# Kernel tuning notes

Hardware: AMD Instinct MI355X
Metric: run time of the kernel (lower is better)

## Reference

```python
import jax, jax.numpy as jnp
import numpy as np

HEADS = 8
IN_C = 256
MDL = 512
N = 4
L = 4096
NE = 65536  # avg degree 16


def setup_inputs() -> dict:
    key = jax.random.key(0)
    ks = jax.random.split(key, 14)
    f32 = jnp.float32
    s = 0.05
    return {
        "queries": jax.random.normal(ks[0], (N, L, IN_C), f32),
        "keys": jax.random.normal(ks[1], (N, L, IN_C), f32),
        "values": jax.random.normal(ks[2], (N, L, IN_C), f32),
        "adj": jax.random.randint(ks[3], (2, NE), 0, L, dtype=jnp.int32),
        "edge_pos_enc": jax.random.normal(ks[4], (N, HEADS, NE), f32),
        "Wq": jax.random.normal(ks[5], (IN_C, MDL), f32) * s,
        "bq": jnp.zeros((MDL,), f32),
        "Wk": jax.random.normal(ks[6], (IN_C, MDL), f32) * s,
        "bk": jnp.zeros((MDL,), f32),
        "Wv": jax.random.normal(ks[7], (IN_C, MDL), f32) * s,
        "bv": jnp.zeros((MDL,), f32),
        "Wo": jax.random.normal(ks[8], (MDL, MDL), f32) * s,
        "bo": jnp.zeros((MDL,), f32),
    }


def reference(queries, keys, values, adj, edge_pos_enc, Wq, bq, Wk, bk, Wv, bv, Wo, bo):
    n, l, _ = queries.shape
    h = HEADS
    e = MDL // h  # per-head dim
    temp = 1.0 / jnp.sqrt(jnp.asarray(e, queries.dtype))
    dst, src = adj[0], adj[1]

    def split(x):  # (n, l, mdl) -> (n*h, l, e)
        return x.reshape(n, l, h, e).transpose(0, 2, 1, 3).reshape(n * h, l, e)

    q = split(queries @ Wq + bq)
    k = split(keys @ Wk + bk)
    v = split(values @ Wv + bv)
    epe = edge_pos_enc.reshape(n * h, NE)

    def head(qh, kh, vh, eh):
        # qh,kh,vh: (l, e); eh: (Ne,)
        scores = temp * (jnp.sum(qh[dst] * kh[src], axis=-1) + eh)  # (Ne,)
        m = jax.ops.segment_max(scores, dst, num_segments=l)
        p = jnp.exp(scores - m[dst])
        z = jax.ops.segment_sum(p, dst, num_segments=l)
        alpha = p / z[dst]  # segment softmax keyed by dst (adj[0])
        return jax.ops.segment_sum(alpha[:, None] * vh[src], dst, num_segments=l)  # (l, e)

    out = jax.vmap(head)(q, k, v, epe)  # (n*h, l, e)
    out = out.reshape(n, h, l, e).transpose(0, 2, 1, 3).reshape(n, l, h * e)
    return out @ Wo + bo
```

## Files before the change

kernel.cpp:

```cpp
#include <hip/hip_runtime.h>
#include <hip/hip_bf16.h>
#include <math.h>
#include <stdint.h>

#define HEADS 8
#define IN_C  256
#define MDL   512
#define NB    4
#define LL    4096
#define NE    65536
#define EDIM  64
#define TEMP  0.125f

typedef __bf16 bf16x8 __attribute__((ext_vector_type(8)));
typedef float  f32x4  __attribute__((ext_vector_type(4)));
typedef short  short8 __attribute__((ext_vector_type(8)));

__device__ __forceinline__ void glds16(const void* g, void* l) {
    __builtin_amdgcn_global_load_lds(
        (const __attribute__((address_space(1))) void*)g,
        (__attribute__((address_space(3))) void*)l, 16, 0, 0);
}

__device__ __forceinline__ short8 cvt8(float4 a, float4 b) {
    union { short8 v; __hip_bfloat16 h[8]; } u;
    u.h[0] = __float2bfloat16(a.x); u.h[1] = __float2bfloat16(a.y);
    u.h[2] = __float2bfloat16(a.z); u.h[3] = __float2bfloat16(a.w);
    u.h[4] = __float2bfloat16(b.x); u.h[5] = __float2bfloat16(b.y);
    u.h[6] = __float2bfloat16(b.z); u.h[7] = __float2bfloat16(b.w);
    return u.v;
}

__global__ __launch_bounds__(256) void gemm_qkv(
    const float* __restrict__ A0, const float* __restrict__ A1,
    const float* __restrict__ A2,
    const __hip_bfloat16* __restrict__ B0, const __hip_bfloat16* __restrict__ B1,
    const __hip_bfloat16* __restrict__ B2,
    const float* __restrict__ b0, const float* __restrict__ b1,
    const float* __restrict__ b2,
    __hip_bfloat16* __restrict__ C0, __hip_bfloat16* __restrict__ C1,
    __hip_bfloat16* __restrict__ C2, int M, int N, int K)
{
    __shared__ __align__(16) __hip_bfloat16 As[128 * 64];
    __shared__ __align__(16) __hip_bfloat16 Bs[128 * 64];

    const int z = blockIdx.z;
    const float* A           = (z == 0) ? A0 : (z == 1) ? A1 : A2;
    const __hip_bfloat16* Bt = (z == 0) ? B0 : (z == 1) ? B1 : B2;
    const float* bias        = (z == 0) ? b0 : (z == 1) ? b1 : b2;
    __hip_bfloat16* C        = (z == 0) ? C0 : (z == 1) ? C1 : C2;

    const int tid  = threadIdx.x;
    const int lane = tid & 63;
    const int w    = tid >> 6;
    const int wr   = w >> 1, wc = w & 1;
    const int bm   = blockIdx.y * 128, bn = blockIdx.x * 128;

    const float*          gA[4];
    const __hip_bfloat16* gB[4];
    __hip_bfloat16* lAw[4];
    __hip_bfloat16* lB[4];
    #pragma unroll
    for (int it = 0; it < 4; it++) {
        int idx  = it * 256 + tid;
        int r    = idx >> 3;
        int cpos = idx & 7;
        int cdat = cpos ^ (r & 7);
        gA[it]  = A  + (size_t)(bm + r) * K + cdat * 8;
        gB[it]  = Bt + (size_t)(bn + r) * K + cdat * 8;
        lAw[it] = As + r * 64 + cpos * 8;
        lB[it]  = Bs + (size_t)(it * 256 + w * 64) * 8;
    }

    int fa[2][4], fb[2][4];
    #pragma unroll
    for (int kk = 0; kk < 2; kk++)
        #pragma unroll
        for (int i = 0; i < 4; i++) {
            int rA = wr * 64 + i * 16 + (lane & 15);
            int gc = kk * 4 + (lane >> 4);
            fa[kk][i] = rA * 64 + (gc ^ (rA & 7)) * 8;
            int rB = wc * 64 + i * 16 + (lane & 15);
            fb[kk][i] = rB * 64 + (gc ^ (rB & 7)) * 8;
        }

    f32x4 acc[4][4] = {};

    for (int k0 = 0; k0 < K; k0 += 64) {
        #pragma unroll
        for (int it = 0; it < 4; it++) glds16(gB[it] + k0, lB[it]);
        #pragma unroll
        for (int it = 0; it < 4; it++) {
            float4 a = *(const float4*)(gA[it] + k0);
            float4 b = *(const float4*)(gA[it] + k0 + 4);
            *(short8*)lAw[it] = cvt8(a, b);
        }
        __syncthreads();

        #pragma unroll
        for (int kk = 0; kk < 2; kk++) {
            bf16x8 av[4], bv[4];
            #pragma unroll
            for (int i = 0; i < 4; i++) av[i] = *(const bf16x8*)(As + fa[kk][i]);
            #pragma unroll
            for (int i = 0; i < 4; i++) bv[i] = *(const bf16x8*)(Bs + fb[kk][i]);
            #pragma unroll
            for (int mi = 0; mi < 4; mi++)
                #pragma unroll
                for (int ni = 0; ni < 4; ni++)
                    acc[mi][ni] = __builtin_amdgcn_mfma_f32_16x16x32_bf16(
                        av[mi], bv[ni], acc[mi][ni], 0, 0, 0);
        }
        __syncthreads();
    }

    #pragma unroll
    for (int mi = 0; mi < 4; mi++) {
        int row = bm + wr * 64 + mi * 16 + (lane >> 4) * 4;
        #pragma unroll
        for (int ni = 0; ni < 4; ni++) {
            int col = bn + wc * 64 + ni * 16 + (lane & 15);
            float bb = bias[col];
            #pragma unroll
            for (int j = 0; j < 4; j++)
                C[(size_t)(row + j) * N + col] = __float2bfloat16(acc[mi][ni][j] + bb);
        }
    }
}

__global__ __launch_bounds__(256) void gemm_out(
    const __hip_bfloat16* __restrict__ A, const __hip_bfloat16* __restrict__ Bt,
    const float* __restrict__ bias, float* __restrict__ C, int M, int N, int K)
{
    __shared__ __align__(16) __hip_bfloat16 As[128 * 64];
    __shared__ __align__(16) __hip_bfloat16 Bs[128 * 64];

    const int tid  = threadIdx.x;
    const int lane = tid & 63;
    const int w    = tid >> 6;
    const int wr   = w >> 1, wc = w & 1;
    const int bm   = blockIdx.y * 128, bn = blockIdx.x * 128;

    const __hip_bfloat16* gA[4];
    const __hip_bfloat16* gB[4];
    __hip_bfloat16* lA[4];
    __hip_bfloat16* lB[4];
    #pragma unroll
    for (int it = 0; it < 4; it++) {
        int idx = it * 256 + tid;
        int r = idx >> 3;
        int c = (idx & 7) ^ (r & 7);
        gA[it] = A  + (size_t)(bm + r) * K + c * 8;
        gB[it] = Bt + (size_t)(bn + r) * K + c * 8;
        lA[it] = As + (size_t)(it * 256 + w * 64) * 8;
        lB[it] = Bs + (size_t)(it * 256 + w * 64) * 8;
    }

    int fa[2][4], fb[2][4];
    #pragma unroll
    for (int kk = 0; kk < 2; kk++)
        #pragma unroll
        for (int i = 0; i < 4; i++) {
            int rA = wr * 64 + i * 16 + (lane & 15);
            int gc = kk * 4 + (lane >> 4);
            fa[kk][i] = rA * 64 + (gc ^ (rA & 7)) * 8;
            int rB = wc * 64 + i * 16 + (lane & 15);
            fb[kk][i] = rB * 64 + (gc ^ (rB & 7)) * 8;
        }

    f32x4 acc[4][4] = {};

    for (int k0 = 0; k0 < K; k0 += 64) {
        #pragma unroll
        for (int it = 0; it < 4; it++) {
            glds16(gA[it] + k0, lA[it]);
            glds16(gB[it] + k0, lB[it]);
        }
        __syncthreads();

        #pragma unroll
        for (int kk = 0; kk < 2; kk++) {
            bf16x8 av[4], bv[4];
            #pragma unroll
            for (int i = 0; i < 4; i++) av[i] = *(const bf16x8*)(As + fa[kk][i]);
            #pragma unroll
            for (int i = 0; i < 4; i++) bv[i] = *(const bf16x8*)(Bs + fb[kk][i]);
            #pragma unroll
            for (int mi = 0; mi < 4; mi++)
                #pragma unroll
                for (int ni = 0; ni < 4; ni++)
                    acc[mi][ni] = __builtin_amdgcn_mfma_f32_16x16x32_bf16(
                        av[mi], bv[ni], acc[mi][ni], 0, 0, 0);
        }
        __syncthreads();
    }

    #pragma unroll
    for (int mi = 0; mi < 4; mi++) {
        int row = bm + wr * 64 + mi * 16 + (lane >> 4) * 4;
        #pragma unroll
        for (int ni = 0; ni < 4; ni++) {
            int col = bn + wc * 64 + ni * 16 + (lane & 15);
            float bb = bias[col];
            #pragma unroll
            for (int j = 0; j < 4; j++)
                C[(size_t)(row + j) * N + col] = acc[mi][ni][j] + bb;
        }
    }
}

__global__ void count_edges(const int* __restrict__ dst, int* __restrict__ counts, int ne) {
    int e = blockIdx.x * blockDim.x + threadIdx.x;
    if (e < ne) atomicAdd(&counts[dst[e]], 1);
}

__global__ __launch_bounds__(1024) void scan_offsets(
    const int* __restrict__ counts, int* __restrict__ offsets,
    int* __restrict__ cursor, int* __restrict__ reorder)
{
    __shared__ int wsum[16];
    __shared__ int bcnt[9], boff[9];
    const int tid  = threadIdx.x;
    const int lane = tid & 63;
    const int wid  = tid >> 6;

    if (tid < 9) bcnt[tid] = 0;

    int c[4];
    int base = tid * 4;
    int s = 0;
    #pragma unroll
    for (int i = 0; i < 4; i++) { c[i] = counts[base + i]; s += c[i]; }

    int v = s;
    #pragma unroll
    for (int off = 1; off < 64; off <<= 1) {
        int t = __shfl_up(v, off);
        if (lane >= off) v += t;
    }
    if (lane == 63) wsum[wid] = v;
    __syncthreads();
    if (wid == 0) {
        int wv = (lane < 16) ? wsum[lane] : 0;
        #pragma unroll
        for (int off = 1; off < 16; off <<= 1) {
            int t = __shfl_up(wv, off);
            if (lane >= off) wv += t;
        }
        if (lane < 16) wsum[lane] = wv;
    }
    __syncthreads();

    int prefix = (wid > 0 ? wsum[wid - 1] : 0) + (v - s);
    int run = prefix;
    int mybk[4];
    #pragma unroll
    for (int i = 0; i < 4; i++) {
        offsets[base + i] = run;
        cursor[base + i]  = run;
        run += c[i];
        int sc = (c[i] + 7) >> 3; if (sc > 8) sc = 8;
        mybk[i] = 8 - sc;
        atomicAdd(&bcnt[mybk[i]], 1);
    }
    if (tid == 1023) offsets[4096] = run;
    __syncthreads();
    if (tid == 0) {
        int acc0 = 0;
        #pragma unroll
        for (int b = 0; b < 9; b++) { boff[b] = acc0; acc0 += bcnt[b]; }
    }
    __syncthreads();
    #pragma unroll
    for (int i = 0; i < 4; i++) {
        int pos = atomicAdd(&boff[mybk[i]], 1);
        reorder[pos] = base + i;
    }
}

__global__ __launch_bounds__(256) void prep(
    const int* __restrict__ dst, const int* __restrict__ srcarr,
    const float* __restrict__ epe, int* __restrict__ cursor,
    int* __restrict__ src_s, float* __restrict__ epe_s,
    const float* __restrict__ Wq, const float* __restrict__ Wk,
    const float* __restrict__ Wv, const float* __restrict__ Wo,
    __hip_bfloat16* __restrict__ Wqt, __hip_bfloat16* __restrict__ Wkt,
    __hip_bfloat16* __restrict__ Wvt, __hip_bfloat16* __restrict__ Wot)
{
    __shared__ float t[32][33];
    const int b = blockIdx.x;

    if (b < 256) {
        int e = b * 256 + threadIdx.x;
        int p = atomicAdd(&cursor[dst[e]], 1);
        src_s[p] = srcarr[e];
        #pragma unroll
        for (int n = 0; n < NB; n++) {
            float4 a2, b2;
            const float* base = epe + (size_t)(n * HEADS) * NE + e;
            a2.x = base[0 * NE]; a2.y = base[1 * NE]; a2.z = base[2 * NE]; a2.w = base[3 * NE];
            b2.x = base[4 * NE]; b2.y = base[5 * NE]; b2.z = base[6 * NE]; b2.w = base[7 * NE];
            float* o = epe_s + ((size_t)n * NE + p) * 8;
            *(float4*)o       = a2;
            *(float4*)(o + 4) = b2;
        }
    } else {
        int bb = b - 256;
        const float* W; __hip_bfloat16* Wt; int K, tt;
        if (bb < 384) {
            int m = bb >> 7; tt = bb & 127; K = IN_C;
            W  = (m == 0) ? Wq  : (m == 1) ? Wk  : Wv;
            Wt = (m == 0) ? Wqt : (m == 1) ? Wkt : Wvt;
        } else {
            tt = bb - 384; K = MDL; W = Wo; Wt = Wot;
        }
        const int N = MDL;
        int bx = (tt & 15) * 32;
        int by = (tt >> 4) * 32;
        int tx = threadIdx.x & 31, ty = threadIdx.x >> 5;
        #pragma unroll
        for (int i = 0; i < 4; i++)
            t[ty + i * 8][tx] = W[(size_t)(by + ty + i * 8) * N + bx + tx];
        __syncthreads();
        #pragma unroll
        for (int i = 0; i < 4; i++)
            Wt[(size_t)(bx + ty + i * 8) * K + by + tx] =
                __float2bfloat16(t[tx][ty + i * 8]);
    }
}

__global__ __launch_bounds__(256) void sparse_score(
    const __hip_bfloat16* __restrict__ Qb, const __hip_bfloat16* __restrict__ Kb,
    const int* __restrict__ src_s, const float* __restrict__ epe_s,
    const int* __restrict__ offsets, const int* __restrict__ reorder,
    float* __restrict__ score_s, float2* __restrict__ mz)
{
    const int lane = threadIdx.x & 63;
    const int wid  = threadIdx.x >> 6;
    const int bid  = blockIdx.x;
    const int xcd  = bid & 7;
    const int n    = xcd >> 1;
    const int base = ((bid >> 3) << 1) | (xcd & 1);
    const int dstn = reorder[(base << 2) | wid];
    const int task = n * LL + dstn;
    const int hg   = lane >> 3;

    const int beg = offsets[dstn];
    const int end = offsets[dstn + 1];
    const int deg = end - beg;
    if (deg == 0) return;

    bf16x8 q8 = *(const bf16x8*)(Qb + (size_t)task * MDL + lane * 8);
    float qf[8];
    #pragma unroll
    for (int j = 0; j < 8; j++) qf[j] = (float)q8[j];

    const __hip_bfloat16* Kn = Kb + (size_t)n * LL * MDL + lane * 8;
    const float* pe_n = epe_s + (size_t)n * NE * 8 + hg;
    float* sc_n = score_s + (size_t)n * NE * 8 + hg;

    float m = -INFINITY, z = 0.0f;

    if (deg <= 64) {
        const int my_src = src_s[beg + ((lane < deg) ? lane : (deg - 1))];

        #pragma unroll
        for (int slot = 0; slot < 8; slot++) {
            const int r0 = slot * 8;
            if (r0 < deg) {
                bf16x8 kk[8];
                #pragma unroll
                for (int j = 0; j < 8; j++) {
                    int s = __shfl(my_src, r0 + j);
                    kk[j] = *(const bf16x8*)(Kn + (size_t)s * MDL);
                }
                const int rel_mine = r0 + (lane & 7);
                float pp = (rel_mine < deg)
                         ? pe_n[(size_t)(beg + rel_mine) * 8] : -INFINITY;

                float p[8];
                #pragma unroll
                for (int j = 0; j < 8; j++) {
                    float d = 0.0f;
                    #pragma unroll
                    for (int dd = 0; dd < 8; dd++)
                        d = fmaf(qf[dd], (float)kk[j][dd], d);
                    p[j] = d;
                }
                float n0, n1, n2, n3, u0, u1, sraw;
                {
                    float a0 = (lane & 1) ? p[1] : p[0];
                    float b0 = (lane & 1) ? p[0] : p[1];
                    n0 = a0 + __shfl_xor(b0, 1);
                    float a1 = (lane & 1) ? p[3] : p[2];
                    float b1 = (lane & 1) ? p[2] : p[3];
                    n1 = a1 + __shfl_xor(b1, 1);
                    float a2 = (lane & 1) ? p[5] : p[4];
                    float b2 = (lane & 1) ? p[4] : p[5];
                    n2 = a2 + __shfl_xor(b2, 1);
                    float a3 = (lane & 1) ? p[7] : p[6];
                    float b3 = (lane & 1) ? p[6] : p[7];
                    n3 = a3 + __shfl_xor(b3, 1);

                    float c0 = (lane & 2) ? n1 : n0;
                    float d0 = (lane & 2) ? n0 : n1;
                    u0 = c0 + __shfl_xor(d0, 2);
                    float c1 = (lane & 2) ? n3 : n2;
                    float d1 = (lane & 2) ? n2 : n3;
                    u1 = c1 + __shfl_xor(d1, 2);

                    float e0 = (lane & 4) ? u1 : u0;
                    float f0 = (lane & 4) ? u0 : u1;
                    sraw = e0 + __shfl_xor(f0, 4);
                }

                float sc_my = TEMP * (sraw + pp);
                if (rel_mine < deg)
                    sc_n[(size_t)(beg + rel_mine) * 8] = sc_my;

                float gm = sc_my;
                gm = fmaxf(gm, __shfl_xor(gm, 1));
                gm = fmaxf(gm, __shfl_xor(gm, 2));
                gm = fmaxf(gm, __shfl_xor(gm, 4));
                float mnew = fmaxf(m, gm);
                float e_my = __expf(sc_my - mnew);
                float gs = e_my;
                gs += __shfl_xor(gs, 1);
                gs += __shfl_xor(gs, 2);
                gs += __shfl_xor(gs, 4);
                z = z * __expf(m - mnew) + gs;
                m = mnew;
            }
        }
    } else {
        for (int i = beg; i < end; i += 4) {
            float sc4[4];
            #pragma unroll
            for (int j = 0; j < 4; j++) {
                int idx = i + j;
                int ok  = idx < end;
                int s   = ok ? src_s[idx] : src_s[beg];
                bf16x8 kk = *(const bf16x8*)(Kn + (size_t)s * MDL);
                float pp = ok ? pe_n[(size_t)idx * 8] : -INFINITY;
                float d = 0.0f;
                #pragma unroll
                for (int dd = 0; dd < 8; dd++) d += qf[dd] * (float)kk[dd];
                d += __shfl_xor(d, 1);
                d += __shfl_xor(d, 2);
                d += __shfl_xor(d, 4);
                sc4[j] = TEMP * (d + pp);
                if (ok && (lane & 7) == 0)
                    sc_n[(size_t)idx * 8] = sc4[j];
            }
            float mb   = fmaxf(fmaxf(sc4[0], sc4[1]), fmaxf(sc4[2], sc4[3]));
            float mnew = fmaxf(m, mb);
            float sc   = __expf(m - mnew);
            float s0 = __expf(sc4[0] - mnew);
            float s1 = __expf(sc4[1] - mnew);
            float s2 = __expf(sc4[2] - mnew);
            float s3 = __expf(sc4[3] - mnew);
            z = z * sc + (s0 + s1 + s2 + s3);
            m = mnew;
        }
    }

    if ((lane & 7) == 0) {
        float2 v; v.x = m; v.y = 1.0f / z;
        mz[(size_t)task * 8 + hg] = v;
    }
}

__global__ __launch_bounds__(256) void sparse_out(
    const __hip_bfloat16* __restrict__ Vb,
    const int* __restrict__ src_s, const float* __restrict__ score_s,
    const int* __restrict__ offsets, const int* __restrict__ reorder,
    const float2* __restrict__ mz, __hip_bfloat16* __restrict__ O)
{
    const int lane = threadIdx.x & 63;
    const int wid  = threadIdx.x >> 6;
    const int bid  = blockIdx.x;
    const int xcd  = bid & 7;
    const int n    = xcd >> 1;
    const int base = ((bid >> 3) << 1) | (xcd & 1);
    const int dstn = reorder[(base << 2) | wid];
    const int task = n * LL + dstn;
    const int hg   = lane >> 3;

    const size_t rowbase = (size_t)task * MDL;
    const int beg = offsets[dstn];
    const int end = offsets[dstn + 1];
    const int deg = end - beg;

    union { short8 v8; __hip_bfloat16 h[8]; } uo;
    if (deg == 0) {
        #pragma unroll
        for (int j = 0; j < 8; j++) uo.h[j] = __float2bfloat16(0.0f);
        *(short8*)(O + rowbase + lane * 8) = uo.v8;
        return;
    }

    float2 mzv = mz[(size_t)task * 8 + hg];
    const float m = mzv.x, zinv = mzv.y;

    const __hip_bfloat16* Vn = Vb + (size_t)n * LL * MDL + lane * 8;
    const float* sc_n = score_s + (size_t)n * NE * 8 + hg;

    float acc[8] = {};

    if (deg <= 64) {
        const int my_src = src_s[beg + ((lane < deg) ? lane : (deg - 1))];

        #pragma unroll
        for (int slot = 0; slot < 8; slot++) {
            const int r0 = slot * 8;
            if (r0 < deg) {
                bf16x8 vv[8];
                #pragma unroll
                for (int j = 0; j < 8; j++) {
                    int s = __shfl(my_src, r0 + j);
                    vv[j] = *(const bf16x8*)(Vn + (size_t)s * MDL);
                }
                const int rel_mine = r0 + (lane & 7);
                float sc = (rel_mine < deg)
                         ? sc_n[(size_t)(beg + rel_mine) * 8] : -INFINITY;
                float a_l = __expf(sc - m) * zinv;
                #pragma unroll
                for (int j = 0; j < 8; j++) {
                    float al = __shfl(a_l, (lane & 56) | j);
                    #pragma unroll
                    for (int dd = 0; dd < 8; dd++)
                        acc[dd] = fmaf(al, (float)vv[j][dd], acc[dd]);
                }
            }
        }
    } else {
        for (int i = beg; i < end; i += 4) {
            #pragma unroll
            for (int j = 0; j < 4; j++) {
                int idx = i + j;
                int ok  = idx < end;
                int s   = ok ? src_s[idx] : src_s[beg];
                bf16x8 vv = *(const bf16x8*)(Vn + (size_t)s * MDL);
                float sc = ok ? sc_n[(size_t)idx * 8] : -INFINITY;
                float al = __expf(sc - m) * zinv;
                #pragma unroll
                for (int dd = 0; dd < 8; dd++)
                    acc[dd] = fmaf(al, (float)vv[dd], acc[dd]);
            }
        }
    }

    #pragma unroll
    for (int j = 0; j < 8; j++) uo.h[j] = __float2bfloat16(acc[j]);
    *(short8*)(O + rowbase + lane * 8) = uo.v8;
}

extern "C" void kernel_launch(void* const* d_in, const int* in_sizes, int n_in,
                              void* d_out, int out_size, void* d_ws, size_t ws_size,
                              hipStream_t stream)
{
    const float* queries = (const float*)d_in[0];
    const float* keys    = (const float*)d_in[1];
    const float* values  = (const float*)d_in[2];
    const int*   adj     = (const int*)d_in[3];
    const float* epe     = (const float*)d_in[4];
    const float* Wq = (const float*)d_in[5];
    const float* bq = (const float*)d_in[6];
    const float* Wk = (const float*)d_in[7];
    const float* bk = (const float*)d_in[8];
    const float* Wv = (const float*)d_in[9];
    const float* bv = (const float*)d_in[10];
    const float* Wo = (const float*)d_in[11];
    const float* bo = (const float*)d_in[12];
    float* out = (float*)d_out;

    const int* dst = adj;
    const int* src = adj + NE;

    const int    M   = NB * LL;
    const size_t NLM = (size_t)M * MDL;

    char* w = (char*)d_ws;
    __hip_bfloat16* Qb  = (__hip_bfloat16*)w; w += NLM * 2;
    __hip_bfloat16* Kb  = (__hip_bfloat16*)w; w += NLM * 2;
    __hip_bfloat16* Vb  = (__hip_bfloat16*)w; w += NLM * 2;
    __hip_bfloat16* Ob  = (__hip_bfloat16*)w; w += NLM * 2;
    __hip_bfloat16* Wqt = (__hip_bfloat16*)w; w += (size_t)MDL * IN_C * 2;
    __hip_bfloat16* Wkt = (__hip_bfloat16*)w; w += (size_t)MDL * IN_C * 2;
    __hip_bfloat16* Wvt = (__hip_bfloat16*)w; w += (size_t)MDL * IN_C * 2;
    __hip_bfloat16* Wot = (__hip_bfloat16*)w; w += (size_t)MDL * MDL * 2;
    int* counts  = (int*)w; w += 4096 * sizeof(int);
    int* offsets = (int*)w; w += 4100 * sizeof(int);
    int* cursor  = (int*)w; w += 4096 * sizeof(int);
    int* reorder = (int*)w; w += 4096 * sizeof(int);
    int*   src_s = (int*)w; w += NE * sizeof(int);
    float* epe_s   = (float*)w;  w += (size_t)NB * NE * 8 * sizeof(float);
    float* score_s = (float*)w;  w += (size_t)NB * NE * 8 * sizeof(float);
    float2* mz     = (float2*)w; w += (size_t)M * 8 * sizeof(float2);

    hipMemsetAsync(counts, 0, 4096 * sizeof(int), stream);
    count_edges<<<NE / 256, 256, 0, stream>>>(dst, counts, NE);
    scan_offsets<<<1, 1024, 0, stream>>>(counts, offsets, cursor, reorder);

    prep<<<896, 256, 0, stream>>>(dst, src, epe, cursor, src_s, epe_s,
                                  Wq, Wk, Wv, Wo, Wqt, Wkt, Wvt, Wot);

    dim3 g3(MDL / 128, M / 128, 3);
    gemm_qkv<<<g3, 256, 0, stream>>>(queries, keys, values, Wqt, Wkt, Wvt,
                                     bq, bk, bv, Qb, Kb, Vb, M, MDL, IN_C);

    sparse_score<<<(NB * LL) / 4, 256, 0, stream>>>(Qb, Kb, src_s, epe_s,
                                                    offsets, reorder, score_s, mz);
    sparse_out<<<(NB * LL) / 4, 256, 0, stream>>>(Vb, src_s, score_s,
                                                  offsets, reorder, mz, Ob);

    dim3 g(MDL / 128, M / 128);
    gemm_out<<<g, 256, 0, stream>>>(Ob, Wot, bo, out, M, MDL, MDL);
}
```

Baseline: 132.0 us.

## Fuse CSR histogram into scan, XCD-aware block mapping, smaller output GEMM tiles

The separate memset, atomic count kernel and scan kernel become one single-block kernel that builds the degree histogram in shared memory and then scans it. Both GEMMs switch to a 1D grid whose block index is remapped so that consecutive row tiles land on the same XCD, which should improve L2 reuse of the A and B tiles. The output GEMM also moves to 64x128 tiles, doubling its block count to 1024 for better occupancy. The single-block histogram serialises 65536 shared atomics on one CU, which may cost more than the launches it removes.

Measured after the change: 116.6 us, median of 2. 1.13x faster.

```diff
diff --git a/kernel.cpp b/kernel.cpp
--- a/kernel.cpp
+++ b/kernel.cpp
@@ -39,12 +39,20 @@
     const float* __restrict__ b0, const float* __restrict__ b1,
     const float* __restrict__ b2,
     __hip_bfloat16* __restrict__ C0, __hip_bfloat16* __restrict__ C1,
-    __hip_bfloat16* __restrict__ C2, int M, int N, int K)
+    __hip_bfloat16* __restrict__ C2)
 {
     __shared__ __align__(16) __hip_bfloat16 As[128 * 64];
     __shared__ __align__(16) __hip_bfloat16 Bs[128 * 64];
 
-    const int z = blockIdx.z;
+    const int K = IN_C, N = MDL;
+    const int lin  = blockIdx.x;
+    const int xcd  = lin & 7;
+    const int t    = lin >> 3;
+    const int z    = t >> 6;
+    const int rest = t & 63;
+    const int bm   = (xcd * 16 + (rest & 15)) * 128;
+    const int bn   = (rest >> 4) * 128;
+
     const float* A           = (z == 0) ? A0 : (z == 1) ? A1 : A2;
     const __hip_bfloat16* Bt = (z == 0) ? B0 : (z == 1) ? B1 : B2;
     const float* bias        = (z == 0) ? b0 : (z == 1) ? b1 : b2;
@@ -54,7 +62,6 @@
     const int lane = tid & 63;
     const int w    = tid >> 6;
     const int wr   = w >> 1, wc = w & 1;
-    const int bm   = blockIdx.y * 128, bn = blockIdx.x * 128;
 
     const float*          gA[4];
     const __hip_bfloat16* gB[4];
@@ -130,63 +137,78 @@
 
 __global__ __launch_bounds__(256) void gemm_out(
     const __hip_bfloat16* __restrict__ A, const __hip_bfloat16* __restrict__ Bt,
-    const float* __restrict__ bias, float* __restrict__ C, int M, int N, int K)
+    const float* __restrict__ bias, float* __restrict__ C)
 {
-    __shared__ __align__(16) __hip_bfloat16 As[128 * 64];
+    __shared__ __align__(16) __hip_bfloat16 As[64 * 64];
     __shared__ __align__(16) __hip_bfloat16 Bs[128 * 64];
+
+    const int K = MDL, N = MDL;
+    const int lin = blockIdx.x;
+    const int xcd = lin & 7;
+    const int t   = lin >> 3;
+    const int bm  = (xcd * 32 + (t & 31)) * 64;
+    const int bn  = (t >> 5) * 128;
 
     const int tid  = threadIdx.x;
     const int lane = tid & 63;
     const int w    = tid >> 6;
     const int wr   = w >> 1, wc = w & 1;
-    const int bm   = blockIdx.y * 128, bn = blockIdx.x * 128;
-
-    const __hip_bfloat16* gA[4];
+
+    const __hip_bfloat16* gA[2];
+    __hip_bfloat16* lA[2];
+    #pragma unroll
+    for (int it = 0; it < 2; it++) {
+        int idx = it * 256 + tid;
+        int r = idx >> 3;
+        int c = (idx & 7) ^ (r & 7);
+        gA[it] = A + (size_t)(bm + r) * K + c * 8;
+        lA[it] = As + (size_t)(it * 256 + w * 64) * 8;
+    }
     const __hip_bfloat16* gB[4];
-    __hip_bfloat16* lA[4];
     __hip_bfloat16* lB[4];
     #pragma unroll
     for (int it = 0; it < 4; it++) {
         int idx = it * 256 + tid;
         int r = idx >> 3;
         int c = (idx & 7) ^ (r & 7);
-        gA[it] = A  + (size_t)(bm + r) * K + c * 8;
         gB[it] = Bt + (size_t)(bn + r) * K + c * 8;
-        lA[it] = As + (size_t)(it * 256 + w * 64) * 8;
         lB[it] = Bs + (size_t)(it * 256 + w * 64) * 8;
     }
 
-    int fa[2][4], fb[2][4];
-    #pragma unroll
-    for (int kk = 0; kk < 2; kk++)
+    int fa[2][2], fb[2][4];
+    #pragma unroll
+    for (int kk = 0; kk < 2; kk++) {
+        int gc = kk * 4 + (lane >> 4);
+        #pragma unroll
+        for (int i = 0; i < 2; i++) {
+            int rA = wr * 32 + i * 16 + (lane & 15);
+            fa[kk][i] = rA * 64 + (gc ^ (rA & 7)) * 8;
+        }
         #pragma unroll
         for (int i = 0; i < 4; i++) {
-            int rA = wr * 64 + i * 16 + (lane & 15);
-            int gc = kk * 4 + (lane >> 4);
-            fa[kk][i] = rA * 64 + (gc ^ (rA & 7)) * 8;
             int rB = wc * 64 + i * 16 + (lane & 15);
             fb[kk][i] = rB * 64 + (gc ^ (rB & 7)) * 8;
         }
-
-    f32x4 acc[4][4] = {};
+    }
+
+    f32x4 acc[2][4] = {};
 
     for (int k0 = 0; k0 < K; k0 += 64) {
         #pragma unroll
-        for (int it = 0; it < 4; it++) {
-            glds16(gA[it] + k0, lA[it]);
-            glds16(gB[it] + k0, lB[it]);
-        }
+        for (int it = 0; it < 2; it++) glds16(gA[it] + k0, lA[it]);
+        #pragma unroll
+        for (int it = 0; it < 4; it++) glds16(gB[it] + k0, lB[it]);
         __syncthreads();
 
         #pragma unroll
         for (int kk = 0; kk < 2; kk++) {
-            bf16x8 av[4], bv[4];
-            #pragma unroll
-            for (int i = 0; i < 4; i++) av[i] = *(const bf16x8*)(As + fa[kk][i]);
+            bf16x8 av[2], bv[4];
+            #pragma unroll
+            for (int i = 0; i < 2; i++) av[i] = *(const bf16x8*)(As + fa[kk][i]);
             #pragma unroll
             for (int i = 0; i < 4; i++) bv[i] = *(const bf16x8*)(Bs + fb[kk][i]);
             #pragma unroll
-            for (int mi = 0; mi < 4; mi++)
+            for (int mi = 0; mi < 2; mi++)
                 #pragma unroll
                 for (int ni = 0; ni < 4; ni++)
                     acc[mi][ni] = __builtin_amdgcn_mfma_f32_16x16x32_bf16(
@@ -196,8 +218,8 @@
     }
 
     #pragma unroll
-    for (int mi = 0; mi < 4; mi++) {
-        int row = bm + wr * 64 + mi * 16 + (lane >> 4) * 4;
+    for (int mi = 0; mi < 2; mi++) {
+        int row = bm + wr * 32 + mi * 16 + (lane >> 4) * 4;
         #pragma unroll
         for (int ni = 0; ni < 4; ni++) {
             int col = bn + wc * 64 + ni * 16 + (lane & 15);
@@ -209,28 +231,38 @@
     }
 }
 
-__global__ void count_edges(const int* __restrict__ dst, int* __restrict__ counts, int ne) {
-    int e = blockIdx.x * blockDim.x + threadIdx.x;
-    if (e < ne) atomicAdd(&counts[dst[e]], 1);
-}
-
-__global__ __launch_bounds__(1024) void scan_offsets(
-    const int* __restrict__ counts, int* __restrict__ offsets,
+__global__ __launch_bounds__(1024) void csr_build(
+    const int* __restrict__ dst, int* __restrict__ offsets,
     int* __restrict__ cursor, int* __restrict__ reorder)
 {
+    __shared__ int hist[4096];
     __shared__ int wsum[16];
     __shared__ int bcnt[9], boff[9];
     const int tid  = threadIdx.x;
     const int lane = tid & 63;
     const int wid  = tid >> 6;
 
+    #pragma unroll
+    for (int i = 0; i < 4; i++) hist[tid + i * 1024] = 0;
     if (tid < 9) bcnt[tid] = 0;
+    __syncthreads();
+
+    const int4* d4 = (const int4*)dst;
+    #pragma unroll
+    for (int i = 0; i < 16; i++) {
+        int4 v = d4[i * 1024 + tid];
+        atomicAdd(&hist[v.x], 1);
+        atomicAdd(&hist[v.y], 1);
+        atomicAdd(&hist[v.z], 1);
+        atomicAdd(&hist[v.w], 1);
+    }
+    __syncthreads();
 
     int c[4];
     int base = tid * 4;
     int s = 0;
     #pragma unroll
-    for (int i = 0; i < 4; i++) { c[i] = counts[base + i]; s += c[i]; }
+    for (int i = 0; i < 4; i++) { c[i] = hist[base + i]; s += c[i]; }
 
     int v = s;
     #pragma unroll
@@ -589,7 +621,6 @@
     __hip_bfloat16* Wkt = (__hip_bfloat16*)w; w += (size_t)MDL * IN_C * 2;
     __hip_bfloat16* Wvt = (__hip_bfloat16*)w; w += (size_t)MDL * IN_C * 2;
     __hip_bfloat16* Wot = (__hip_bfloat16*)w; w += (size_t)MDL * MDL * 2;
-    int* counts  = (int*)w; w += 4096 * sizeof(int);
     int* offsets = (int*)w; w += 4100 * sizeof(int);
     int* cursor  = (int*)w; w += 4096 * sizeof(int);
     int* reorder = (int*)w; w += 4096 * sizeof(int);
@@ -598,22 +629,18 @@
     float* score_s = (float*)w;  w += (size_t)NB * NE * 8 * sizeof(float);
     float2* mz     = (float2*)w; w += (size_t)M * 8 * sizeof(float2);
 
-    hipMemsetAsync(counts, 0, 4096 * sizeof(int), stream);
-    count_edges<<<NE / 256, 256, 0, stream>>>(dst, counts, NE);
-    scan_offsets<<<1, 1024, 0, stream>>>(counts, offsets, cursor, reorder);
+    csr_build<<<1, 1024, 0, stream>>>(dst, offsets, cursor, reorder);
 
     prep<<<896, 256, 0, stream>>>(dst, src, epe, cursor, src_s, epe_s,
                                   Wq, Wk, Wv, Wo, Wqt, Wkt, Wvt, Wot);
 
-    dim3 g3(MDL / 128, M / 128, 3);
-    gemm_qkv<<<g3, 256, 0, stream>>>(queries, keys, values, Wqt, Wkt, Wvt,
-                                     bq, bk, bv, Qb, Kb, Vb, M, MDL, IN_C);
+    gemm_qkv<<<1536, 256, 0, stream>>>(queries, keys, values, Wqt, Wkt, Wvt,
+                                       bq, bk, bv, Qb, Kb, Vb);
 
     sparse_score<<<(NB * LL) / 4, 256, 0, stream>>>(Qb, Kb, src_s, epe_s,
                                                     offsets, reorder, score_s, mz);
     sparse_out<<<(NB * LL) / 4, 256, 0, stream>>>(Vb, src_s, score_s,
                                                   offsets, reorder, mz, Ob);
 
-    dim3 g(MDL / 128, M / 128);
-    gemm_out<<<g, 256, 0, stream>>>(Ob, Wot, bo, out, M, MDL, MDL);
-}
+    gemm_out<<<1024, 256, 0, stream>>>(Ob, Wot, bo, out);
+}
```
